# Kernel tuning notes

Measured on AMD Instinct MI355X. Metric: run time of the kernel, lower is better.

## Reference

```python
import jax, jax.numpy as jnp
import numpy as np
from jax import lax

DT = 0.5
DX = 100.0 / 48.0
DU, DV, FF, KK = 0.2, 0.1, 0.025, 0.055


def _laplace_filter_5x5x5():
    # Fourth-order accurate 3D Laplacian stencil: sum of three 1D stencils
    # [-1/12, 4/3, -5/2, 4/3, -1/12] placed along each axis through the center.
    s = np.array([-1.0 / 12, 4.0 / 3, -5.0 / 2, 4.0 / 3, -1.0 / 12], dtype=np.float32)
    w = np.zeros((5, 5, 5), dtype=np.float32)
    w[:, 2, 2] += s
    w[2, :, 2] += s
    w[2, 2, :] += s
    return jnp.asarray(w.reshape(1, 1, 5, 5, 5))


def setup_inputs() -> dict:
    key = jax.random.key(0)
    T, C, Y, X, Z = 50, 2, 100, 100, 100
    output = jax.random.normal(key, (T, C, Y, X, Z), dtype=jnp.float32)
    laplace_filter = _laplace_filter_5x5x5()
    return {"output": output, "laplace_filter": laplace_filter}


def _laplace(x, w):
    # x: [N,1,Y,X,Z], w: [1,1,5,5,5]; VALID conv (crop 2 on each spatial side)
    y = lax.conv_general_dilated(
        x, w, window_strides=(1, 1, 1), padding="VALID",
        dimension_numbers=("NCDHW", "OIDHW", "NCDHW"))
    return y / (DX * DX)


def reference(output, laplace_filter):
    u_full = output[:, 0:1]  # [T,1,Y,X,Z]
    v_full = output[:, 1:2]

    laplace_u = _laplace(u_full[:-2], laplace_filter)  # [T-2,1,Y-4,X-4,Z-4]
    laplace_v = _laplace(v_full[:-2], laplace_filter)

    ui = u_full[:, :, 2:-2, 2:-2, 2:-2]  # interior, [T,1,...]
    vi = v_full[:, :, 2:-2, 2:-2, 2:-2]

    # Conv1d filter [-1,1,0] along time == forward difference (u[t+1]-u[t])/dt
    u_t = (ui[1:-1] - ui[:-2]) / DT  # [T-2,1,...]
    v_t = (vi[1:-1] - vi[:-2]) / DT

    u = ui[:-2]
    v = vi[:-2]

    uv2 = u * v * v
    f_u = DU * laplace_u - uv2 + FF * (1.0 - u) - u_t
    f_v = DV * laplace_v + uv2 - (FF + KK) * v - v_t
    return (f_u, f_v)
```

## Files before the change

### kernel.cpp

```cpp
#include <hip/hip_runtime.h>


#define N_OUT (48 * 96 * 96 * 96)

__global__ __launch_bounds__(256) void grayscott_kernel(
    const float* __restrict__ in, float* __restrict__ out) {
  const int idx = blockIdx.x * 256 + threadIdx.x;

  int oz = idx % 96;
  int tmp = idx / 96;
  int ox = tmp % 96;
  tmp /= 96;
  int oy = tmp % 96;
  int t = tmp / 96;

  const int iz = oz + 2;
  const int ix = ox + 2;
  const int iy = oy + 2;

  const int base = t * 2000000 + iy * 10000 + ix * 100 + iz;
  const float* __restrict__ u = in + base;
  const float* __restrict__ v = in + base + 1000000;

  const float c0 = -1.0f / 12.0f;
  const float c1 = 4.0f / 3.0f;
  const float cc = -7.5f;
  const float inv_dx2 = 0.2304f;

  const float uc = u[0];
  const float vc = v[0];

  float lap_u = cc * uc
      + c1 * (u[1] + u[-1] + u[100] + u[-100] + u[10000] + u[-10000])
      + c0 * (u[2] + u[-2] + u[200] + u[-200] + u[20000] + u[-20000]);
  float lap_v = cc * vc
      + c1 * (v[1] + v[-1] + v[100] + v[-100] + v[10000] + v[-10000])
      + c0 * (v[2] + v[-2] + v[200] + v[-200] + v[20000] + v[-20000]);

  const float un = u[2000000];
  const float vn = v[2000000];

  lap_u *= inv_dx2;
  lap_v *= inv_dx2;

  const float uv2 = uc * vc * vc;
  const float f_u = 0.2f * lap_u - uv2 + 0.025f * (1.0f - uc) - (un - uc) * 2.0f;
  const float f_v = 0.1f * lap_v + uv2 - 0.08f * vc - (vn - vc) * 2.0f;

  out[idx] = f_u;
  out[idx + N_OUT] = f_v;
}

extern "C" void kernel_launch(void* const* d_in, const int* in_sizes, int n_in,
                              void* d_out, int out_size, void* d_ws, size_t ws_size,
                              hipStream_t stream) {
  const float* in = (const float*)d_in[0];
  float* out = (float*)d_out;
  const int nblocks = N_OUT / 256;
  grayscott_kernel<<<dim3(nblocks), dim3(256), 0, stream>>>(in, out);
}
```

Before: 808.7 us.

## Process two z-points per thread with float2 loads, XCD block swizzle, nontemporal stores

Each thread now computes two adjacent z outputs, using 8-byte vector loads for every stencil tap and sharing the overlapping z-neighbours between the two points. Block indices are remapped so that consecutive chunks of the grid land on the same one of 8 groups, which is meant to improve L2 locality across the MI355X's chiplets. Outputs are written with nontemporal float2 stores to avoid polluting cache. The number of load instructions per output drops, at the cost of more registers per thread and half as many threads.

Result: no change. 804.6 us (-0.5%).

```diff
diff --git a/kernel.cpp b/kernel.cpp
--- a/kernel.cpp
+++ b/kernel.cpp
@@ -2,19 +2,26 @@
 
 
 #define N_OUT (48 * 96 * 96 * 96)
+#define NPAIR (N_OUT / 2)
+#define NBLK  (NPAIR / 256)
+#define CHUNK (NBLK / 8)
+
+typedef float f2 __attribute__((ext_vector_type(2)));
 
 __global__ __launch_bounds__(256) void grayscott_kernel(
     const float* __restrict__ in, float* __restrict__ out) {
-  const int idx = blockIdx.x * 256 + threadIdx.x;
+  const int b = blockIdx.x;
+  const int wb = (b & 7) * CHUNK + (b >> 3);
+  const int vid = wb * 256 + (int)threadIdx.x;
 
-  int oz = idx % 96;
-  int tmp = idx / 96;
-  int ox = tmp % 96;
+  const int ozp = vid % 48;
+  int tmp = vid / 48;
+  const int ox = tmp % 96;
   tmp /= 96;
-  int oy = tmp % 96;
-  int t = tmp / 96;
+  const int oy = tmp % 96;
+  const int t = tmp / 96;
 
-  const int iz = oz + 2;
+  const int iz = ozp * 2 + 2;
   const int ix = ox + 2;
   const int iy = oy + 2;
 
@@ -22,33 +29,71 @@
   const float* __restrict__ u = in + base;
   const float* __restrict__ v = in + base + 1000000;
 
+#define LD2(p) (*(const f2*)(p))
+
+  const f2 uzm  = LD2(u - 2);
+  const f2 ucc  = LD2(u);
+  const f2 uzp  = LD2(u + 2);
+  const f2 uxm1 = LD2(u - 100);
+  const f2 uxp1 = LD2(u + 100);
+  const f2 uxm2 = LD2(u - 200);
+  const f2 uxp2 = LD2(u + 200);
+  const f2 uym1 = LD2(u - 10000);
+  const f2 uyp1 = LD2(u + 10000);
+  const f2 uym2 = LD2(u - 20000);
+  const f2 uyp2 = LD2(u + 20000);
+  const f2 un   = LD2(u + 2000000);
+
+  const f2 vzm  = LD2(v - 2);
+  const f2 vcc  = LD2(v);
+  const f2 vzp  = LD2(v + 2);
+  const f2 vxm1 = LD2(v - 100);
+  const f2 vxp1 = LD2(v + 100);
+  const f2 vxm2 = LD2(v - 200);
+  const f2 vxp2 = LD2(v + 200);
+  const f2 vym1 = LD2(v - 10000);
+  const f2 vyp1 = LD2(v + 10000);
+  const f2 vym2 = LD2(v - 20000);
+  const f2 vyp2 = LD2(v + 20000);
+  const f2 vn   = LD2(v + 2000000);
+
   const float c0 = -1.0f / 12.0f;
   const float c1 = 4.0f / 3.0f;
   const float cc = -7.5f;
   const float inv_dx2 = 0.2304f;
 
-  const float uc = u[0];
-  const float vc = v[0];
+  f2 fu, fv;
 
-  float lap_u = cc * uc
-      + c1 * (u[1] + u[-1] + u[100] + u[-100] + u[10000] + u[-10000])
-      + c0 * (u[2] + u[-2] + u[200] + u[-200] + u[20000] + u[-20000]);
-  float lap_v = cc * vc
-      + c1 * (v[1] + v[-1] + v[100] + v[-100] + v[10000] + v[-10000])
-      + c0 * (v[2] + v[-2] + v[200] + v[-200] + v[20000] + v[-20000]);
+  {
+    float lap_u = cc * ucc.x
+        + c1 * (ucc.y + uzm.y + uxp1.x + uxm1.x + uyp1.x + uym1.x)
+        + c0 * (uzp.x + uzm.x + uxp2.x + uxm2.x + uyp2.x + uym2.x);
+    float lap_v = cc * vcc.x
+        + c1 * (vcc.y + vzm.y + vxp1.x + vxm1.x + vyp1.x + vym1.x)
+        + c0 * (vzp.x + vzm.x + vxp2.x + vxm2.x + vyp2.x + vym2.x);
+    lap_u *= inv_dx2;
+    lap_v *= inv_dx2;
+    const float uv2 = ucc.x * vcc.x * vcc.x;
+    fu.x = 0.2f * lap_u - uv2 + 0.025f * (1.0f - ucc.x) - (un.x - ucc.x) * 2.0f;
+    fv.x = 0.1f * lap_v + uv2 - 0.08f * vcc.x - (vn.x - vcc.x) * 2.0f;
+  }
 
-  const float un = u[2000000];
-  const float vn = v[2000000];
+  {
+    float lap_u = cc * ucc.y
+        + c1 * (uzp.x + ucc.x + uxp1.y + uxm1.y + uyp1.y + uym1.y)
+        + c0 * (uzp.y + uzm.y + uxp2.y + uxm2.y + uyp2.y + uym2.y);
+    float lap_v = cc * vcc.y
+        + c1 * (vzp.x + vcc.x + vxp1.y + vxm1.y + vyp1.y + vym1.y)
+        + c0 * (vzp.y + vzm.y + vxp2.y + vxm2.y + vyp2.y + vym2.y);
+    lap_u *= inv_dx2;
+    lap_v *= inv_dx2;
+    const float uv2 = ucc.y * vcc.y * vcc.y;
+    fu.y = 0.2f * lap_u - uv2 + 0.025f * (1.0f - ucc.y) - (un.y - ucc.y) * 2.0f;
+    fv.y = 0.1f * lap_v + uv2 - 0.08f * vcc.y - (vn.y - vcc.y) * 2.0f;
+  }
 
-  lap_u *= inv_dx2;
-  lap_v *= inv_dx2;
-
-  const float uv2 = uc * vc * vc;
-  const float f_u = 0.2f * lap_u - uv2 + 0.025f * (1.0f - uc) - (un - uc) * 2.0f;
-  const float f_v = 0.1f * lap_v + uv2 - 0.08f * vc - (vn - vc) * 2.0f;
-
-  out[idx] = f_u;
-  out[idx + N_OUT] = f_v;
+  __builtin_nontemporal_store(fu, (f2*)(out + 2 * vid));
+  __builtin_nontemporal_store(fv, (f2*)(out + 2 * vid + N_OUT));
 }
 
 extern "C" void kernel_launch(void* const* d_in, const int* in_sizes, int n_in,
@@ -56,6 +101,5 @@
                               hipStream_t stream) {
   const float* in = (const float*)d_in[0];
   float* out = (float*)d_out;
-  const int nblocks = N_OUT / 256;
-  grayscott_kernel<<<dim3(nblocks), dim3(256), 0, stream>>>(in, out);
+  grayscott_kernel<<<dim3(NBLK), dim3(256), 0, stream>>>(in, out);
 }
```

## Vectorize stencil to four z-outputs per thread with wide loads and nontemporal stores

Applied to the files above, without the earlier changes.

Each thread now computes four consecutive z outputs, using float4 loads for the z neighborhood and float2 loads for the x, y and time neighbors, then writes results with nontemporal float4 stores. Block indices are remapped with an XCD-style interleave so consecutive work lands on the same chiplet. This cuts the number of load instructions and the index arithmetic per output, and keeps output writes from polluting the cache. In exchange it raises register pressure and gives fewer threads, and it relies on 8- and 16-byte aligned addresses, which hold because base is a multiple of 4.

Result: faster. 743.8 us (-8.0%).

```diff
diff --git a/kernel.cpp b/kernel.cpp
--- a/kernel.cpp
+++ b/kernel.cpp
@@ -2,53 +2,107 @@
 
 
 #define N_OUT (48 * 96 * 96 * 96)
+#define NTHRD (N_OUT / 4)
+#define NBLK  (NTHRD / 256)
+#define CHUNK (NBLK / 8)
+
+typedef float f2 __attribute__((ext_vector_type(2)));
+typedef float f4 __attribute__((ext_vector_type(4)));
+
+#define LD4(p) (*(const f4*)(p))
+#define LD2(p) (*(const f2*)(p))
 
 __global__ __launch_bounds__(256) void grayscott_kernel(
     const float* __restrict__ in, float* __restrict__ out) {
-  const int idx = blockIdx.x * 256 + threadIdx.x;
+  const int b = blockIdx.x;
+  const int wb = (b & 7) * CHUNK + (b >> 3);
+  const int vid = wb * 256 + (int)threadIdx.x;
 
-  int oz = idx % 96;
-  int tmp = idx / 96;
-  int ox = tmp % 96;
+  const int zq = vid % 24;
+  int tmp = vid / 24;
+  const int ox = tmp % 96;
   tmp /= 96;
-  int oy = tmp % 96;
-  int t = tmp / 96;
+  const int oy = tmp % 96;
+  const int t = tmp / 96;
 
-  const int iz = oz + 2;
   const int ix = ox + 2;
   const int iy = oy + 2;
 
-  const int base = t * 2000000 + iy * 10000 + ix * 100 + iz;
+  const int base = t * 2000000 + iy * 10000 + ix * 100 + 4 * zq;
   const float* __restrict__ u = in + base;
   const float* __restrict__ v = in + base + 1000000;
+
+  const f4 uza = LD4(u);          const f4 vza = LD4(v);
+  const f4 uzb = LD4(u + 4);      const f4 vzb = LD4(v + 4);
+
+  const f2 uxm1a = LD2(u - 100 + 2),   uxm1b = LD2(u - 100 + 4);
+  const f2 uxp1a = LD2(u + 100 + 2),   uxp1b = LD2(u + 100 + 4);
+  const f2 uxm2a = LD2(u - 200 + 2),   uxm2b = LD2(u - 200 + 4);
+  const f2 uxp2a = LD2(u + 200 + 2),   uxp2b = LD2(u + 200 + 4);
+  const f2 uym1a = LD2(u - 10000 + 2), uym1b = LD2(u - 10000 + 4);
+  const f2 uyp1a = LD2(u + 10000 + 2), uyp1b = LD2(u + 10000 + 4);
+  const f2 uym2a = LD2(u - 20000 + 2), uym2b = LD2(u - 20000 + 4);
+  const f2 uyp2a = LD2(u + 20000 + 2), uyp2b = LD2(u + 20000 + 4);
+  const f2 utna  = LD2(u + 2000000 + 2), utnb = LD2(u + 2000000 + 4);
+
+  const f2 vxm1a = LD2(v - 100 + 2),   vxm1b = LD2(v - 100 + 4);
+  const f2 vxp1a = LD2(v + 100 + 2),   vxp1b = LD2(v + 100 + 4);
+  const f2 vxm2a = LD2(v - 200 + 2),   vxm2b = LD2(v - 200 + 4);
+  const f2 vxp2a = LD2(v + 200 + 2),   vxp2b = LD2(v + 200 + 4);
+  const f2 vym1a = LD2(v - 10000 + 2), vym1b = LD2(v - 10000 + 4);
+  const f2 vyp1a = LD2(v + 10000 + 2), vyp1b = LD2(v + 10000 + 4);
+  const f2 vym2a = LD2(v - 20000 + 2), vym2b = LD2(v - 20000 + 4);
+  const f2 vyp2a = LD2(v + 20000 + 2), vyp2b = LD2(v + 20000 + 4);
+  const f2 vtna  = LD2(v + 2000000 + 2), vtnb = LD2(v + 2000000 + 4);
+
+  const float uzv[8] = {uza.x, uza.y, uza.z, uza.w, uzb.x, uzb.y, uzb.z, uzb.w};
+  const float vzv[8] = {vza.x, vza.y, vza.z, vza.w, vzb.x, vzb.y, vzb.z, vzb.w};
+
+  const float uxm1[4] = {uxm1a.x, uxm1a.y, uxm1b.x, uxm1b.y};
+  const float uxp1[4] = {uxp1a.x, uxp1a.y, uxp1b.x, uxp1b.y};
+  const float uxm2[4] = {uxm2a.x, uxm2a.y, uxm2b.x, uxm2b.y};
+  const float uxp2[4] = {uxp2a.x, uxp2a.y, uxp2b.x, uxp2b.y};
+  const float uym1[4] = {uym1a.x, uym1a.y, uym1b.x, uym1b.y};
+  const float uyp1[4] = {uyp1a.x, uyp1a.y, uyp1b.x, uyp1b.y};
+  const float uym2[4] = {uym2a.x, uym2a.y, uym2b.x, uym2b.y};
+  const float uyp2[4] = {uyp2a.x, uyp2a.y, uyp2b.x, uyp2b.y};
+  const float utn[4]  = {utna.x,  utna.y,  utnb.x,  utnb.y};
+
+  const float vxm1[4] = {vxm1a.x, vxm1a.y, vxm1b.x, vxm1b.y};
+  const float vxp1[4] = {vxp1a.x, vxp1a.y, vxp1b.x, vxp1b.y};
+  const float vxm2[4] = {vxm2a.x, vxm2a.y, vxm2b.x, vxm2b.y};
+  const float vxp2[4] = {vxp2a.x, vxp2a.y, vxp2b.x, vxp2b.y};
+  const float vym1[4] = {vym1a.x, vym1a.y, vym1b.x, vym1b.y};
+  const float vyp1[4] = {vyp1a.x, vyp1a.y, vyp1b.x, vyp1b.y};
+  const float vym2[4] = {vym2a.x, vym2a.y, vym2b.x, vym2b.y};
+  const float vyp2[4] = {vyp2a.x, vyp2a.y, vyp2b.x, vyp2b.y};
+  const float vtn[4]  = {vtna.x,  vtna.y,  vtnb.x,  vtnb.y};
 
   const float c0 = -1.0f / 12.0f;
   const float c1 = 4.0f / 3.0f;
   const float cc = -7.5f;
   const float inv_dx2 = 0.2304f;
 
-  const float uc = u[0];
-  const float vc = v[0];
+  f4 fu, fv;
+#pragma unroll
+  for (int j = 0; j < 4; ++j) {
+    const float uc = uzv[j + 2];
+    const float vc = vzv[j + 2];
+    float lap_u = cc * uc
+        + c1 * (uzv[j + 1] + uzv[j + 3] + uxp1[j] + uxm1[j] + uyp1[j] + uym1[j])
+        + c0 * (uzv[j] + uzv[j + 4] + uxp2[j] + uxm2[j] + uyp2[j] + uym2[j]);
+    float lap_v = cc * vc
+        + c1 * (vzv[j + 1] + vzv[j + 3] + vxp1[j] + vxm1[j] + vyp1[j] + vym1[j])
+        + c0 * (vzv[j] + vzv[j + 4] + vxp2[j] + vxm2[j] + vyp2[j] + vym2[j]);
+    lap_u *= inv_dx2;
+    lap_v *= inv_dx2;
+    const float uv2 = uc * vc * vc;
+    fu[j] = 0.2f * lap_u - uv2 + 0.025f * (1.0f - uc) - (utn[j] - uc) * 2.0f;
+    fv[j] = 0.1f * lap_v + uv2 - 0.08f * vc - (vtn[j] - vc) * 2.0f;
+  }
 
-  float lap_u = cc * uc
-      + c1 * (u[1] + u[-1] + u[100] + u[-100] + u[10000] + u[-10000])
-      + c0 * (u[2] + u[-2] + u[200] + u[-200] + u[20000] + u[-20000]);
-  float lap_v = cc * vc
-      + c1 * (v[1] + v[-1] + v[100] + v[-100] + v[10000] + v[-10000])
-      + c0 * (v[2] + v[-2] + v[200] + v[-200] + v[20000] + v[-20000]);
-
-  const float un = u[2000000];
-  const float vn = v[2000000];
-
-  lap_u *= inv_dx2;
-  lap_v *= inv_dx2;
-
-  const float uv2 = uc * vc * vc;
-  const float f_u = 0.2f * lap_u - uv2 + 0.025f * (1.0f - uc) - (un - uc) * 2.0f;
-  const float f_v = 0.1f * lap_v + uv2 - 0.08f * vc - (vn - vc) * 2.0f;
-
-  out[idx] = f_u;
-  out[idx + N_OUT] = f_v;
+  __builtin_nontemporal_store(fu, (f4*)(out + 4 * vid));
+  __builtin_nontemporal_store(fv, (f4*)(out + 4 * vid + N_OUT));
 }
 
 extern "C" void kernel_launch(void* const* d_in, const int* in_sizes, int n_in,
@@ -56,6 +110,5 @@
                               hipStream_t stream) {
   const float* in = (const float*)d_in[0];
   float* out = (float*)d_out;
-  const int nblocks = N_OUT / 256;
-  grayscott_kernel<<<dim3(nblocks), dim3(256), 0, stream>>>(in, out);
+  grayscott_kernel<<<dim3(NBLK), dim3(256), 0, stream>>>(in, out);
 }
```
